# Kernel optimization log

Hardware: AMD Instinct MI355X
Metric: run time of the kernel (lower is better)

## Reference

```python
import jax, jax.numpy as jnp
import numpy as np

EPS = 1e-12
HEADS = 8
STRIDE = 4  # saccade_stride default

def conv1x1(x, w, b=None):
    # 1x1 conv == channel-mixing einsum; x: (B,C,H,W), w: (O,C)
    y = jnp.einsum('bchw,oc->bohw', x, w)
    if b is not None:
        y = y + b[None, :, None, None]
    return y

def ln2d(x, g, b, eps=1e-5):
    # LayerNorm across channel dim per spatial location (population variance)
    mu = x.mean(axis=1, keepdims=True)
    var = x.var(axis=1, keepdims=True)
    xn = (x - mu) / jnp.sqrt(var + eps)
    return xn * g[None, :, None, None] + b[None, :, None, None]

def l2norm(x):
    n = jnp.linalg.norm(x, axis=-1, keepdims=True)
    return x / jnp.maximum(n, EPS)

def cos_attn(q, k, v, scale):
    # q:(B,h,Q,d) k,v:(B,h,K,d); QK-normalized (cosine) attention
    logits = jnp.einsum('bhqd,bhkd->bhqk', l2norm(q), l2norm(k)) * scale
    a = jax.nn.softmax(logits, axis=-1)
    return jnp.einsum('bhqk,bhkd->bhqd', a, v)

def gqa(x, qkv_w, proj_w, proj_b):
    # grouped-query attention; group loop == per-head full attention
    B, C, H, W = x.shape
    hd = C // HEADS
    seq = H * W
    qkv = conv1x1(x, qkv_w).reshape(B, 3, HEADS, hd, seq)
    q, k, v = (jnp.swapaxes(qkv[:, i], -1, -2) for i in range(3))  # (B,h,seq,hd)
    out = cos_attn(q, k, v, hd ** -0.5)
    out = jnp.swapaxes(out, -1, -2).reshape(B, C, H, W)
    return conv1x1(out, proj_w, proj_b)

def block_forward(x, g1, b1, loc_qkv_w, loc_proj_w, loc_proj_b,
                  glob_qkv_w, glob_proj_w, glob_proj_b,
                  fuse_w1, fuse_b1, fuse_w2, fuse_b2,
                  glat, blat, latents, qlat_w, kvx_w, qx_w, kvlat_w,
                  lat_proj_w, lat_proj_b, g2, b2,
                  ffn_w1, ffn_b1, ffn_w2, ffn_b2):
    B, C, H, W = x.shape
    hd = C // HEADS
    seq = H * W
    scale = hd ** -0.5
    # --- BioAttentionFusion branch ---
    xn = ln2d(x, g1, b1)
    local = gqa(xn, loc_qkv_w, loc_proj_w, loc_proj_b)
    xc = xn.reshape(B, C, H // STRIDE, STRIDE, W // STRIDE, STRIDE).mean(axis=(3, 5))
    g = gqa(xc, glob_qkv_w, glob_proj_w, glob_proj_b)
    g = jax.image.resize(g, (B, C, H, W), method='bilinear')  # align_corners=False semantics
    f = conv1x1(jnp.concatenate([local, g], axis=1), fuse_w1, fuse_b1)
    f = conv1x1(jax.nn.gelu(f, approximate=False), fuse_w2, fuse_b2)
    x = x + f
    # --- LatentMixer branch ---
    xn = ln2d(x, glat, blat)
    L = latents.shape[-1]
    lat = jnp.broadcast_to(latents, (B, C, 1, L))
    ql = jnp.swapaxes(conv1x1(lat, qlat_w).reshape(B, HEADS, hd, L), -1, -2)
    kx, vx = jnp.split(conv1x1(xn, kvx_w), 2, axis=1)
    kx = jnp.swapaxes(kx.reshape(B, HEADS, hd, seq), -1, -2)
    vx = jnp.swapaxes(vx.reshape(B, HEADS, hd, seq), -1, -2)
    lat_read = cos_attn(ql, kx, vx, scale)  # latents read features
    lat_read = jnp.swapaxes(lat_read, -1, -2).reshape(B, C, 1, L)
    qx = jnp.swapaxes(conv1x1(xn, qx_w).reshape(B, HEADS, hd, seq), -1, -2)
    kl, vl = jnp.split(conv1x1(lat_read, kvlat_w), 2, axis=1)
    kl = jnp.swapaxes(kl.reshape(B, HEADS, hd, L), -1, -2)
    vl = jnp.swapaxes(vl.reshape(B, HEADS, hd, L), -1, -2)
    xw = cos_attn(qx, kl, vl, scale)  # features read latents back
    xw = jnp.swapaxes(xw, -1, -2).reshape(B, C, H, W)
    x = x + conv1x1(xw, lat_proj_w, lat_proj_b)
    # --- FFN branch ---
    xn = ln2d(x, g2, b2)
    h = jax.nn.gelu(conv1x1(xn, ffn_w1, ffn_b1), approximate=False)
    return x + conv1x1(h, ffn_w2, ffn_b2)

def setup_inputs() -> dict:
    key = jax.random.key(0)
    ks = jax.random.split(key, 24)
    B, C, H, W, L = 2, 128, 48, 48, 16
    def w(k, shape, s=0.02):
        return jax.random.normal(k, shape, jnp.float32) * s
    return {
        'x': jax.random.normal(ks[0], (B, C, H, W), jnp.float32),
        'g1': jnp.ones((C,), jnp.float32), 'b1': jnp.zeros((C,), jnp.float32),
        'loc_qkv_w': w(ks[1], (3 * C, C)),
        'loc_proj_w': w(ks[2], (C, C)), 'loc_proj_b': jnp.zeros((C,), jnp.float32),
        'glob_qkv_w': w(ks[3], (3 * C, C)),
        'glob_proj_w': w(ks[4], (C, C)), 'glob_proj_b': jnp.zeros((C,), jnp.float32),
        'fuse_w1': w(ks[5], (C, 2 * C)), 'fuse_b1': jnp.zeros((C,), jnp.float32),
        'fuse_w2': w(ks[6], (C, C)), 'fuse_b2': jnp.zeros((C,), jnp.float32),
        'glat': jnp.ones((C,), jnp.float32), 'blat': jnp.zeros((C,), jnp.float32),
        'latents': w(ks[7], (1, C, 1, L), 0.02),
        'qlat_w': w(ks[8], (C, C)), 'kvx_w': w(ks[9], (2 * C, C)),
        'qx_w': w(ks[10], (C, C)), 'kvlat_w': w(ks[11], (2 * C, C)),
        'lat_proj_w': w(ks[12], (C, C)), 'lat_proj_b': jnp.zeros((C,), jnp.float32),
        'g2': jnp.ones((C,), jnp.float32), 'b2': jnp.zeros((C,), jnp.float32),
        'ffn_w1': w(ks[13], (4 * C, C)), 'ffn_b1': jnp.zeros((4 * C,), jnp.float32),
        'ffn_w2': w(ks[14], (C, 4 * C)), 'ffn_b2': jnp.zeros((C,), jnp.float32),
    }

def reference(x, g1, b1, loc_qkv_w, loc_proj_w, loc_proj_b,
              glob_qkv_w, glob_proj_w, glob_proj_b,
              fuse_w1, fuse_b1, fuse_w2, fuse_b2,
              glat, blat, latents, qlat_w, kvx_w, qx_w, kvlat_w,
              lat_proj_w, lat_proj_b, g2, b2,
              ffn_w1, ffn_b1, ffn_w2, ffn_b2):
    return block_forward(x, g1, b1, loc_qkv_w, loc_proj_w, loc_proj_b,
                         glob_qkv_w, glob_proj_w, glob_proj_b,
                         fuse_w1, fuse_b1, fuse_w2, fuse_b2,
                         glat, blat, latents, qlat_w, kvx_w, qx_w, kvlat_w,
                         lat_proj_w, lat_proj_b, g2, b2,
                         ffn_w1, ffn_b1, ffn_w2, ffn_b2)
```

## Files before the change

kernel.cpp:

```cpp
#include <hip/hip_runtime.h>
#include <hip/hip_bf16.h>

typedef __hip_bfloat16 bf16;
typedef _Float16 f16;
typedef _Float16 f16x4 __attribute__((ext_vector_type(4)));
typedef float f32x4 __attribute__((ext_vector_type(4)));

#define HD 16
#define TK 128
#define KP 20
#define MINIT (-1e30f)

__device__ __forceinline__ float b2f(bf16 v){ return __bfloat162float(v); }
__device__ __forceinline__ float gelu_f(float x){ return 0.5f*x*(1.0f+erff(x*0.70710678118654752f)); }
__device__ __forceinline__ float rdv(const void* p, size_t i, bool bf){
  return bf ? b2f(((const bf16*)p)[i]) : ((const float*)p)[i];
}
__device__ __forceinline__ float4 ld4f(const void* p, size_t i, bool bf){
  if (bf){
    const bf16* q = (const bf16*)p + i;
    return make_float4(b2f(q[0]), b2f(q[1]), b2f(q[2]), b2f(q[3]));
  }
  return *(const float4*)((const float*)p + i);
}

__global__ void detect_k(const void* __restrict__ x, float* __restrict__ flag){
  if (blockIdx.x != 0) return;
  int l = threadIdx.x;
  const float* xf = (const float*)x;
  const bf16*  xb = (const bf16*)x;
  float sF = 0.f, sB = 0.f;
  for (int i = l; i < 512; i += 64){ float v = fabsf(xf[i]);      if (!(v < 1e30f)) v = 1e30f; sF += v; }
  for (int i = l; i < 1024; i += 64){ float v = fabsf(b2f(xb[i])); if (!(v < 1e30f)) v = 1e30f; sB += v; }
  #pragma unroll
  for (int o = 32; o; o >>= 1){ sF += __shfl_xor(sF, o); sB += __shfl_xor(sB, o); }
  if (l == 0){
    float mF = sF/512.f, mB = sB/1024.f;
    float dF = fabsf(logf(fmaxf(mF, 1e-30f)));
    float dB = fabsf(logf(fmaxf(mB, 1e-30f)));
    *flag = (dB <= dF) ? 1.0f : 0.0f;
  }
}

__global__ void cvt_k(const void* __restrict__ in, float* __restrict__ out, int n,
                      const float* __restrict__ flagp){
  bool bf = *flagp > 0.5f;
  int i = blockIdx.x*blockDim.x + threadIdx.x;
  if (i < n) out[i] = rdv(in, i, bf);
}

__global__ __launch_bounds__(256) void ln2dw_k(
    const float* __restrict__ x, const void* __restrict__ g,
    const void* __restrict__ b, float* __restrict__ y,
    int C, int HW, const float* __restrict__ flagp)
{
  __shared__ float redS[16][16];
  __shared__ float redQ[16][16];
  bool bf = *flagp > 0.5f;
  int t = threadIdx.x, pix = t & 15, sub = t >> 4;
  int p  = blockIdx.x*16 + pix;
  int bb = blockIdx.y;
  const float* xb = x + (size_t)bb*C*HW + p;
  float xv[8];
  float s = 0.f, s2 = 0.f;
  #pragma unroll
  for (int i = 0; i < 8; i++){
    float v = xb[(size_t)(sub*8 + i)*HW];
    xv[i] = v; s += v; s2 += v*v;
  }
  redS[sub][pix] = s; redQ[sub][pix] = s2;
  __syncthreads();
  float st = 0.f, qt = 0.f;
  #pragma unroll
  for (int j = 0; j < 16; j++){ st += redS[j][pix]; qt += redQ[j][pix]; }
  float mu  = st / (float)C;
  float var = fmaxf(qt / (float)C - mu*mu, 0.f);
  float inv = rsqrtf(var + 1e-5f);
  float* yb = y + (size_t)bb*C*HW + p;
  #pragma unroll
  for (int i = 0; i < 8; i++){
    int c = sub*8 + i;
    yb[(size_t)c*HW] = (xv[i] - mu)*inv*rdv(g, c, bf) + rdv(b, c, bf);
  }
}

__global__ void normk_k(float* __restrict__ KV, long kbs, int koff, int NK){
  int p = blockIdx.x*blockDim.x + threadIdx.x;
  if (p >= NK) return;
  int h = blockIdx.y, bb = blockIdx.z;
  float* base = KV + (size_t)bb*kbs + (size_t)(koff + h*16)*NK + p;
  float v[16]; float s = 0.f;
  #pragma unroll
  for (int d = 0; d < 16; d++){ v[d] = base[(size_t)d*NK]; s += v[d]*v[d]; }
  float iv = 1.f / fmaxf(sqrtf(s), 1e-12f);
  #pragma unroll
  for (int d = 0; d < 16; d++) base[(size_t)d*NK] = v[d]*iv;
}

__global__ void conv1x1_k(const float* __restrict__ in1, long in1_bs, int C1,
                          const float* __restrict__ in2, long in2_bs, int C2,
                          const void* __restrict__ w, const void* __restrict__ bias,
                          const float* __restrict__ res,
                          void* __restrict__ out, int to_out, int O, int NP, int act,
                          int raw1, const float* __restrict__ flagp){
  bool bf = *flagp > 0.5f;
  int p = blockIdx.x*blockDim.x + threadIdx.x;
  if (p >= NP) return;
  int o = blockIdx.y, bb = blockIdx.z;
  size_t wrow = (size_t)o*(C1 + C2);
  float acc = bias ? rdv(bias, o, bf) : 0.f;
  if (raw1){
    for (int c = 0; c < C1; c++)
      acc += rdv(w, wrow + c, bf) * rdv(in1, (size_t)bb*in1_bs + (size_t)c*NP + p, bf);
  } else {
    const float* i1 = in1 + (size_t)bb*in1_bs + p;
    for (int c = 0; c < C1; c++) acc += rdv(w, wrow + c, bf) * i1[(size_t)c*NP];
  }
  if (in2){
    const float* i2 = in2 + (size_t)bb*in2_bs + p;
    for (int c = 0; c < C2; c++) acc += rdv(w, wrow + C1 + c, bf) * i2[(size_t)c*NP];
  }
  if (act == 1) acc = gelu_f(acc);
  if (res) acc += res[((size_t)bb*O + o)*NP + p];
  size_t oi = ((size_t)bb*O + o)*NP + p;
  if (to_out){
    if (bf) ((bf16*)out)[oi] = __float2bfloat16(acc);
    else    ((float*)out)[oi] = acc;
  } else {
    ((float*)out)[oi] = acc;
  }
}

__global__ __launch_bounds__(64) void convmfma_k(
    const float* __restrict__ in1, long in1_bs, int C1,
    const float* __restrict__ in2, long in2_bs, int C2,
    const void* __restrict__ w, const void* __restrict__ bias,
    const float* __restrict__ res, void* __restrict__ out, int to_out,
    int O, int NP, int act, int nlo, int nhi, const float* __restrict__ flagp)
{
  bool bf = *flagp > 0.5f;
  int lane = threadIdx.x;
  int lm = lane & 15, lg = lane >> 4;
  int p0 = blockIdx.x*16, o0 = blockIdx.y*16, bb = blockIdx.z;
  int CW = C1 + C2;
  f32x4 d; d[0]=0.f; d[1]=0.f; d[2]=0.f; d[3]=0.f;
  const float* x1 = in1 + (size_t)bb*in1_bs + p0 + lm;
  const float* x2 = in2 ? (in2 + (size_t)bb*in2_bs + p0 + lm) : nullptr;
  #pragma unroll 8
  for (int kc = 0; kc < CW; kc += 16){
    f16x4 xb;
    #pragma unroll
    for (int i = 0; i < 4; i++){
      int c = kc + lg*4 + i;
      float v = (c < C1) ? x1[(size_t)c*NP] : x2[(size_t)(c - C1)*NP];
      xb[i] = (f16)v;
    }
    float4 wv = ld4f(w, (size_t)(o0 + lm)*CW + kc + lg*4, bf);
    f16x4 wa; wa[0]=(f16)wv.x; wa[1]=(f16)wv.y; wa[2]=(f16)wv.z; wa[3]=(f16)wv.w;
    d = __builtin_amdgcn_mfma_f32_16x16x16f16(wa, xb, d, 0, 0, 0);
  }
  if (o0 >= nlo && o0 < nhi){
    float ss = d[0]*d[0] + d[1]*d[1] + d[2]*d[2] + d[3]*d[3];
    ss += __shfl_xor(ss, 16); ss += __shfl_xor(ss, 32);
    float iv = 1.f / fmaxf(sqrtf(ss), 1e-12f);
    d[0]*=iv; d[1]*=iv; d[2]*=iv; d[3]*=iv;
  }
  #pragma unroll
  for (int r = 0; r < 4; r++){
    int o = o0 + lg*4 + r;
    float v = d[r] + (bias ? rdv(bias, o, bf) : 0.f);
    if (act == 1) v = gelu_f(v);
    size_t oi = ((size_t)bb*O + o)*NP + p0 + lm;
    if (res) v += res[oi];
    if (to_out && bf) ((bf16*)out)[oi] = __float2bfloat16(v);
    else              ((float*)out)[oi] = v;
  }
}

__global__ __launch_bounds__(512) void flat_mfma_k(
    const float* __restrict__ Q, long qbs, int qoff,
    const float* __restrict__ KV, long kbs, int koff, int voff,
    float* __restrict__ Out, long obs, int NQ, int NK, float scale)
{
  __shared__ float OS[8*4*16*17];
  __shared__ float LS[8*4*16];
  int t = threadIdx.x, lane = t & 63, wv = t >> 6;
  int h = blockIdx.y, bb = blockIdx.z;
  int qb = blockIdx.x*64;
  int lm = lane & 15, lg = lane >> 4;
  const float* qp  = Q  + (size_t)bb*qbs;
  const float* kvb = KV + (size_t)bb*kbs;
  f16x4 qf[4];
  #pragma unroll
  for (int qt = 0; qt < 4; qt++){
    float qv[4]; float ss = 0.f;
    #pragma unroll
    for (int i = 0; i < 4; i++){
      qv[i] = qp[(size_t)(qoff + h*16 + lg*4 + i)*NQ + qb + qt*16 + lm];
      ss += qv[i]*qv[i];
    }
    ss += __shfl_xor(ss, 16); ss += __shfl_xor(ss, 32);
    float inv = scale / fmaxf(sqrtf(ss), 1e-12f);
    #pragma unroll
    for (int i = 0; i < 4; i++) qf[qt][i] = (f16)(qv[i]*inv);
  }
  f32x4 of[4];
  float ls[4];
  #pragma unroll
  for (int qt = 0; qt < 4; qt++){
    of[qt][0]=0.f; of[qt][1]=0.f; of[qt][2]=0.f; of[qt][3]=0.f; ls[qt]=0.f;
  }
  int chunk = NK >> 3;
  int p0 = wv*chunk, p1 = p0 + chunk;
  const float* kc = kvb + (size_t)(koff + h*16)*NK;
  const float* vc = kvb + (size_t)(voff + h*16)*NK;
  for (int pos = p0; pos < p1; pos += 16){
    f16x4 kf;
    #pragma unroll
    for (int i = 0; i < 4; i++)
      kf[i] = (f16)kc[(size_t)(lg*4 + i)*NK + pos + lm];
    float4 vvv = *(const float4*)&vc[(size_t)lm*NK + pos + lg*4];
    f16x4 vf; vf[0]=(f16)vvv.x; vf[1]=(f16)vvv.y; vf[2]=(f16)vvv.z; vf[3]=(f16)vvv.w;
    #pragma unroll
    for (int qt = 0; qt < 4; qt++){
      f32x4 s; s[0]=0.f; s[1]=0.f; s[2]=0.f; s[3]=0.f;
      s = __builtin_amdgcn_mfma_f32_16x16x16f16(kf, qf[qt], s, 0, 0, 0);
      f16x4 pf;
      #pragma unroll
      for (int r = 0; r < 4; r++){
        float pp = __expf(s[r]);
        ls[qt] += pp;
        pf[r] = (f16)pp;
      }
      of[qt] = __builtin_amdgcn_mfma_f32_16x16x16f16(vf, pf, of[qt], 0, 0, 0);
    }
  }
  #pragma unroll
  for (int qt = 0; qt < 4; qt++){
    ls[qt] += __shfl_xor(ls[qt], 16);
    ls[qt] += __shfl_xor(ls[qt], 32);
    #pragma unroll
    for (int r = 0; r < 4; r++)
      OS[((wv*4 + qt)*16 + lm)*17 + lg*4 + r] = of[qt][r];
    if (lg == 0) LS[(wv*4 + qt)*16 + lm] = ls[qt];
  }
  __syncthreads();
  #pragma unroll
  for (int rep = 0; rep < 2; rep++){
    int o = t + rep*512;
    int d = o >> 6, qq = o & 63;
    int qt = qq >> 4, q = qq & 15;
    float acc = 0.f, lsum = 0.f;
    #pragma unroll
    for (int w = 0; w < 8; w++){
      acc  += OS[((w*4 + qt)*16 + q)*17 + d];
      lsum += LS[(w*4 + qt)*16 + q];
    }
    Out[(size_t)bb*obs + (size_t)(h*16 + d)*NQ + qb + qq] = acc / fmaxf(lsum, 1e-30f);
  }
}

__global__ __launch_bounds__(256) void attn4_k(
    const float* __restrict__ Q, long qbs, int qoff,
    const float* __restrict__ KV, long kbs, int koff, int voff,
    float* __restrict__ Out, long obs, int NQ, int NK, float scale)
{
  __shared__ __align__(16) float Ks[TK*KP];
  __shared__ __align__(16) float Vs[TK*KP];
  int tid = threadIdx.x;
  int sub = tid & 3;
  int h = blockIdx.y, bb = blockIdx.z;
  int qi = blockIdx.x*64 + (tid >> 2);
  bool qv = qi < NQ;
  float qn[4] = {0,0,0,0}, acc[4] = {0,0,0,0};
  float l = 0.f;
  if (qv){
    float s = 0.f;
    #pragma unroll
    for (int j = 0; j < 4; j++){
      qn[j] = Q[(size_t)bb*qbs + (size_t)(qoff + h*16 + sub*4 + j)*NQ + qi];
      s += qn[j]*qn[j];
    }
    s += __shfl_xor(s, 1); s += __shfl_xor(s, 2);
    float inv = scale / fmaxf(sqrtf(s), 1e-12f);
    #pragma unroll
    for (int j = 0; j < 4; j++) qn[j] *= inv;
  }
  for (int k0 = 0; k0 < NK; k0 += TK){
    int lim = min(TK, NK - k0);
    for (int i = tid; i < 16*TK; i += 256){
      int pos = i & (TK-1), d = i >> 7;
      if (pos < lim){
        Ks[pos*KP + d] = KV[(size_t)bb*kbs + (size_t)(koff + h*16 + d)*NK + k0 + pos];
        Vs[pos*KP + d] = KV[(size_t)bb*kbs + (size_t)(voff + h*16 + d)*NK + k0 + pos];
      }
    }
    __syncthreads();
    for (int pos = 0; pos < lim; pos++){
      float4 k4 = *(const float4*)&Ks[pos*KP + sub*4];
      float dd = qn[0]*k4.x + qn[1]*k4.y + qn[2]*k4.z + qn[3]*k4.w;
      dd += __shfl_xor(dd, 1); dd += __shfl_xor(dd, 2);
      float pp = __expf(dd);
      l += pp;
      float4 v4 = *(const float4*)&Vs[pos*KP + sub*4];
      acc[0] += pp*v4.x;
      acc[1] += pp*v4.y;
      acc[2] += pp*v4.z;
      acc[3] += pp*v4.w;
    }
    __syncthreads();
  }
  if (qv){
    float li = 1.f / fmaxf(l, 1e-30f);
    #pragma unroll
    for (int j = 0; j < 4; j++)
      Out[(size_t)bb*obs + (size_t)(h*16 + sub*4 + j)*NQ + qi] = acc[j]*li;
  }
}

__global__ void latpart_k(const float* __restrict__ ql, const float* __restrict__ kvx,
                          long kbs, float* __restrict__ part, int NK, int S){
  int s = blockIdx.x, h = blockIdx.y, bb = blockIdx.z;
  int t = threadIdx.x;
  int q = t & 15, sub = (t >> 4) & 3;
  float qn[16]; float ss = 0.f;
  #pragma unroll
  for (int d = 0; d < 16; d++){
    qn[d] = ql[(size_t)bb*2048 + (size_t)(h*16+d)*16 + q];
    ss += qn[d]*qn[d];
  }
  float inv = 0.25f / fmaxf(sqrtf(ss), 1e-12f);
  #pragma unroll
  for (int d = 0; d < 16; d++) qn[d] *= inv;
  float l = 0.f, acc[16];
  #pragma unroll
  for (int d = 0; d < 16; d++) acc[d] = 0.f;
  int chunk = NK / S, c4 = chunk >> 2;
  int k0 = s*chunk + sub*c4, k1 = k0 + c4;
  const float* kb = kvx + (size_t)bb*kbs;
  for (int pos = k0; pos < k1; pos++){
    float dot = 0.f;
    #pragma unroll
    for (int d = 0; d < 16; d++) dot += qn[d]*kb[(size_t)(h*16+d)*NK + pos];
    float pp = __expf(dot);
    l += pp;
    #pragma unroll
    for (int d = 0; d < 16; d++)
      acc[d] += pp*kb[(size_t)(128 + h*16+d)*NK + pos];
  }
  l += __shfl_xor(l, 16); l += __shfl_xor(l, 32);
  #pragma unroll
  for (int d = 0; d < 16; d++){
    acc[d] += __shfl_xor(acc[d], 16);
    acc[d] += __shfl_xor(acc[d], 32);
  }
  if ((t >> 4) == 0){
    size_t idx = (size_t)((((bb*8 + h)*16 + q)*S) + s)*18;
    part[idx] = l;
    #pragma unroll
    for (int d = 0; d < 16; d++) part[idx+1+d] = acc[d];
  }
}

__global__ void latcomb_k(const float* __restrict__ part, float* __restrict__ latr, int S){
  int i = blockIdx.x*blockDim.x + threadIdx.x;
  int d = i & 15, q = (i >> 4) & 15, h = (i >> 8) & 7, bb = i >> 11;
  size_t base = (size_t)(((bb*8 + h)*16 + q)*S)*18;
  float L = 0.f, a = 0.f;
  for (int s = 0; s < S; s++){
    const float* ps = part + base + (size_t)s*18;
    L += ps[0];
    a += ps[1+d];
  }
  latr[(size_t)bb*2048 + (size_t)(h*16+d)*16 + q] = a / fmaxf(L, 1e-30f);
}

__global__ void pool4_k(const float* __restrict__ xn, float* __restrict__ xc){
  int i = blockIdx.x*blockDim.x + threadIdx.x;
  if (i >= 2*128*144) return;
  int pc = i % 144; int bc = i / 144;
  int hc = pc / 12, wc = pc % 12;
  const float* s = xn + (size_t)bc*2304 + hc*4*48 + wc*4;
  float acc = 0.f;
  #pragma unroll
  for (int r = 0; r < 4; r++)
    #pragma unroll
    for (int c2 = 0; c2 < 4; c2++) acc += s[r*48 + c2];
  xc[i] = acc * 0.0625f;
}

__global__ void ups_k(const float* __restrict__ g, float* __restrict__ out){
  int i = blockIdx.x*blockDim.x + threadIdx.x;
  if (i >= 2*128*2304) return;
  int p = i % 2304; int bc = i / 2304;
  int h = p / 48, w = p % 48;
  float sh = h*0.25f - 0.375f;
  float sw = w*0.25f - 0.375f;
  float fh0 = floorf(sh), fw0 = floorf(sw);
  float fh = sh - fh0, fw = sw - fw0;
  int h0 = (int)fh0, w0 = (int)fw0;
  int h0c = min(11, max(0, h0)),   h1c = min(11, max(0, h0+1));
  int w0c = min(11, max(0, w0)),   w1c = min(11, max(0, w0+1));
  const float* s = g + (size_t)bc*144;
  float v00 = s[h0c*12 + w0c], v01 = s[h0c*12 + w1c];
  float v10 = s[h1c*12 + w0c], v11 = s[h1c*12 + w1c];
  out[i] = (1.f-fh)*((1.f-fw)*v00 + fw*v01) + fh*((1.f-fw)*v10 + fw*v11);
}

extern "C" void kernel_launch(void* const* d_in, const int* in_sizes, int n_in,
                              void* d_out, int out_size, void* d_ws, size_t ws_size,
                              hipStream_t stream){
  const int B = 2, C = 128, HW = 2304;
  const void* x_in        = d_in[0];
  const void* g1          = d_in[1];
  const void* b1          = d_in[2];
  const void* loc_qkv_w   = d_in[3];
  const void* loc_proj_w  = d_in[4];
  const void* loc_proj_b  = d_in[5];
  const void* glob_qkv_w  = d_in[6];
  const void* glob_proj_w = d_in[7];
  const void* glob_proj_b = d_in[8];
  const void* fuse_w1     = d_in[9];
  const void* fuse_b1     = d_in[10];
  const void* fuse_w2     = d_in[11];
  const void* fuse_b2     = d_in[12];
  const void* glat        = d_in[13];
  const void* blat        = d_in[14];
  const void* latents     = d_in[15];
  const void* qlat_w      = d_in[16];
  const void* kvx_w       = d_in[17];
  const void* qx_w        = d_in[18];
  const void* kvlat_w     = d_in[19];
  const void* lat_proj_w  = d_in[20];
  const void* lat_proj_b  = d_in[21];
  const void* g2          = d_in[22];
  const void* b2          = d_in[23];
  const void* ffn_w1      = d_in[24];
  const void* ffn_b1      = d_in[25];
  const void* ffn_w2      = d_in[26];
  const void* ffn_b2      = d_in[27];

  float* ws = (float*)d_ws;
  float* P  = ws + 0;
  float* N  = ws + 589824;
  float* A  = ws + 1179648;
  float* Q  = ws + 1769472;
  float* FLAG = ws + 4128768;

  float* qkv   = Q;
  float* L     = Q + 1769472;
  float* xc    = Q;
  float* qkvc  = Q + 36864;
  float* gatt  = Q + 147456;
  float* gproj = Q + 184320;
  float* kvx   = Q;
  float* qlat  = Q + 1181696;
  float* latr  = Q + 1185792;
  float* kvlat = Q + 1189888;
  float* part  = Q + 1198080;
  float* ffh   = Q;

  dim3 blk(256);
  dim3 blk512(512);
  dim3 blk64(64);

  detect_k<<<1, 64, 0, stream>>>(x_in, FLAG);
  cvt_k<<<2304, blk, 0, stream>>>(x_in, P, 589824, FLAG);

  ln2dw_k<<<dim3(144,B), blk, 0, stream>>>(P, g1, b1, N, C, HW, FLAG);
  convmfma_k<<<dim3(144,24,B), blk64, 0, stream>>>(N,(long)C*HW,C, nullptr,0,0, loc_qkv_w,nullptr,nullptr, qkv,0,384,HW,0, 128,256, FLAG);
  flat_mfma_k<<<dim3(36,8,B), blk512, 0, stream>>>(qkv,(long)384*HW,0, qkv,(long)384*HW,128,256, A,(long)C*HW, HW,HW,0.25f);
  convmfma_k<<<dim3(144,8,B), blk64, 0, stream>>>(A,(long)C*HW,C, nullptr,0,0, loc_proj_w,loc_proj_b,nullptr, L,0,C,HW,0, 0,0, FLAG);
  pool4_k<<<144, blk, 0, stream>>>(N, xc);
  conv1x1_k<<<dim3(1,384,B), blk, 0, stream>>>(xc,(long)C*144,C, nullptr,0,0, glob_qkv_w,nullptr,nullptr, qkvc,0,384,144,0, 0, FLAG);
  normk_k<<<dim3(1,8,B), blk, 0, stream>>>(qkvc, (long)384*144, 128, 144);
  attn4_k<<<dim3(3,8,B), blk, 0, stream>>>(qkvc,(long)384*144,0, qkvc,(long)384*144,128,256, gatt,(long)C*144, 144,144,0.25f);
  conv1x1_k<<<dim3(1,128,B), blk, 0, stream>>>(gatt,(long)C*144,C, nullptr,0,0, glob_proj_w,glob_proj_b,nullptr, gproj,0,C,144,0, 0, FLAG);
  ups_k<<<2304, blk, 0, stream>>>(gproj, A);
  convmfma_k<<<dim3(144,8,B), blk64, 0, stream>>>(L,(long)C*HW,C, A,(long)C*HW,C, fuse_w1,fuse_b1,nullptr, N,0,C,HW,1, 0,0, FLAG);
  convmfma_k<<<dim3(144,8,B), blk64, 0, stream>>>(N,(long)C*HW,C, nullptr,0,0, fuse_w2,fuse_b2,P, P,0,C,HW,0, 0,0, FLAG);

  ln2dw_k<<<dim3(144,B), blk, 0, stream>>>(P, glat, blat, N, C, HW, FLAG);
  convmfma_k<<<dim3(144,16,B), blk64, 0, stream>>>(N,(long)C*HW,C, nullptr,0,0, kvx_w,nullptr,nullptr, kvx,0,256,HW,0, 0,128, FLAG);
  convmfma_k<<<dim3(144,8,B), blk64, 0, stream>>>(N,(long)C*HW,C, nullptr,0,0, qx_w,nullptr,nullptr, A,0,C,HW,0, 0,0, FLAG);
  conv1x1_k<<<dim3(1,128,B), blk, 0, stream>>>((const float*)latents,0L,C, nullptr,0,0, qlat_w,nullptr,nullptr, qlat,0,C,16,0, 1, FLAG);
  latpart_k<<<dim3(48,8,B), 64, 0, stream>>>(qlat, kvx, (long)256*HW, part, HW, 48);
  latcomb_k<<<16, blk, 0, stream>>>(part, latr, 48);
  conv1x1_k<<<dim3(1,256,B), blk, 0, stream>>>(latr,(long)C*16,C, nullptr,0,0, kvlat_w,nullptr,nullptr, kvlat,0,256,16,0, 0, FLAG);
  normk_k<<<dim3(1,8,B), blk, 0, stream>>>(kvlat, (long)256*16, 0, 16);
  attn4_k<<<dim3(36,8,B), blk, 0, stream>>>(A,(long)C*HW,0, kvlat,(long)256*16,0,128, N,(long)C*HW, HW,16,0.25f);
  convmfma_k<<<dim3(144,8,B), blk64, 0, stream>>>(N,(long)C*HW,C, nullptr,0,0, lat_proj_w,lat_proj_b,P, P,0,C,HW,0, 0,0, FLAG);

  ln2dw_k<<<dim3(144,B), blk, 0, stream>>>(P, g2, b2, N, C, HW, FLAG);
  convmfma_k<<<dim3(144,32,B), blk64, 0, stream>>>(N,(long)C*HW,C, nullptr,0,0, ffn_w1,ffn_b1,nullptr, ffh,0,512,HW,1, 0,0, FLAG);
  convmfma_k<<<dim3(144,8,B), blk64, 0, stream>>>(ffh,(long)512*HW,512, nullptr,0,0, ffn_w2,ffn_b2,P, d_out,1,C,HW,0, 0,0, FLAG);
}
```

Measured before the change: 462.7 us.

## Fuse layernorm, pooling, upsample and k-norm into MFMA conv kernel

Extends the MFMA 1x1-conv kernel with optional prologues: a per-pixel channel layernorm computed via lane shuffles, 4x4 average pooling of the input, and bilinear upsampling of the second input. It also routes the small global and latent convolutions through the MFMA kernel, using its built-in L2-normalisation of the key rows. Together this removes the separate ln2d, pool, upsample, normk and scalar conv launches and their intermediate buffers. In exchange, the layernorm statistics are recomputed in every output-channel block (up to 32 times for the FFN), the pooling reads 16 values per input element, and the unroll factor drops to 4.

```diff
diff --git a/kernel.cpp b/kernel.cpp
--- a/kernel.cpp
+++ b/kernel.cpp
@@ -82,19 +82,6 @@
     int c = sub*8 + i;
     yb[(size_t)c*HW] = (xv[i] - mu)*inv*rdv(g, c, bf) + rdv(b, c, bf);
   }
-}
-
-__global__ void normk_k(float* __restrict__ KV, long kbs, int koff, int NK){
-  int p = blockIdx.x*blockDim.x + threadIdx.x;
-  if (p >= NK) return;
-  int h = blockIdx.y, bb = blockIdx.z;
-  float* base = KV + (size_t)bb*kbs + (size_t)(koff + h*16)*NK + p;
-  float v[16]; float s = 0.f;
-  #pragma unroll
-  for (int d = 0; d < 16; d++){ v[d] = base[(size_t)d*NK]; s += v[d]*v[d]; }
-  float iv = 1.f / fmaxf(sqrtf(s), 1e-12f);
-  #pragma unroll
-  for (int d = 0; d < 16; d++) base[(size_t)d*NK] = v[d]*iv;
 }
 
 __global__ void conv1x1_k(const float* __restrict__ in1, long in1_bs, int C1,
@@ -136,23 +123,71 @@
     const float* __restrict__ in2, long in2_bs, int C2,
     const void* __restrict__ w, const void* __restrict__ bias,
     const float* __restrict__ res, void* __restrict__ out, int to_out,
-    int O, int NP, int act, int nlo, int nhi, const float* __restrict__ flagp)
+    int O, int NP, int act, int nlo, int nhi,
+    int lnf, const void* __restrict__ lng, const void* __restrict__ lnb,
+    int pool, int ups2, const float* __restrict__ flagp)
 {
   bool bf = *flagp > 0.5f;
   int lane = threadIdx.x;
   int lm = lane & 15, lg = lane >> 4;
   int p0 = blockIdx.x*16, o0 = blockIdx.y*16, bb = blockIdx.z;
   int CW = C1 + C2;
+  const float* x1 = in1 + (size_t)bb*in1_bs + p0 + lm;
+  const float* x2b = in2 ? (in2 + (size_t)bb*in2_bs) : nullptr;
+  float fh = 0.f, fw = 0.f; int i00=0, i01=0, i10=0, i11=0;
+  if (ups2){
+    int p = p0 + lm; int hh = p/48, ww = p%48;
+    float sh = hh*0.25f - 0.375f, sw = ww*0.25f - 0.375f;
+    float fh0 = floorf(sh), fw0 = floorf(sw);
+    fh = sh - fh0; fw = sw - fw0;
+    int h0 = (int)fh0, w0 = (int)fw0;
+    int h0c = min(11, max(0, h0)), h1c = min(11, max(0, h0+1));
+    int w0c = min(11, max(0, w0)), w1c = min(11, max(0, w0+1));
+    i00 = h0c*12 + w0c; i01 = h0c*12 + w1c; i10 = h1c*12 + w0c; i11 = h1c*12 + w1c;
+  }
+  const float* pN = nullptr;
+  if (pool){
+    int pc = p0 + lm; int hc = pc/12, wc = pc%12;
+    pN = in1 + (size_t)bb*in1_bs + hc*192 + wc*4;
+  }
+  float mu = 0.f, linv = 0.f;
+  if (lnf){
+    float s = 0.f, s2 = 0.f;
+    for (int c = lg; c < CW; c += 4){ float v = x1[(size_t)c*NP]; s += v; s2 += v*v; }
+    s  += __shfl_xor(s, 16);  s  += __shfl_xor(s, 32);
+    s2 += __shfl_xor(s2, 16); s2 += __shfl_xor(s2, 32);
+    mu = s / (float)CW;
+    float var = fmaxf(s2/(float)CW - mu*mu, 0.f);
+    linv = rsqrtf(var + 1e-5f);
+  }
   f32x4 d; d[0]=0.f; d[1]=0.f; d[2]=0.f; d[3]=0.f;
-  const float* x1 = in1 + (size_t)bb*in1_bs + p0 + lm;
-  const float* x2 = in2 ? (in2 + (size_t)bb*in2_bs + p0 + lm) : nullptr;
-  #pragma unroll 8
+  #pragma unroll 4
   for (int kc = 0; kc < CW; kc += 16){
     f16x4 xb;
     #pragma unroll
     for (int i = 0; i < 4; i++){
       int c = kc + lg*4 + i;
-      float v = (c < C1) ? x1[(size_t)c*NP] : x2[(size_t)(c - C1)*NP];
+      float v;
+      if (pool){
+        const float* s = pN + (size_t)c*2304;
+        float a = 0.f;
+        #pragma unroll
+        for (int r = 0; r < 4; r++)
+          #pragma unroll
+          for (int cc = 0; cc < 4; cc++) a += s[r*48 + cc];
+        v = a * 0.0625f;
+      } else if (c < C1){
+        v = x1[(size_t)c*NP];
+        if (lnf) v = (v - mu)*linv*rdv(lng, c, bf) + rdv(lnb, c, bf);
+      } else {
+        int c2 = c - C1;
+        if (ups2){
+          const float* s = x2b + (size_t)c2*144;
+          v = (1.f-fh)*((1.f-fw)*s[i00] + fw*s[i01]) + fh*((1.f-fw)*s[i10] + fw*s[i11]);
+        } else {
+          v = x2b[(size_t)c2*NP + p0 + lm];
+        }
+      }
       xb[i] = (f16)v;
     }
     float4 wv = ld4f(w, (size_t)(o0 + lm)*CW + kc + lg*4, bf);
@@ -373,38 +408,6 @@
     a += ps[1+d];
   }
   latr[(size_t)bb*2048 + (size_t)(h*16+d)*16 + q] = a / fmaxf(L, 1e-30f);
-}
-
-__global__ void pool4_k(const float* __restrict__ xn, float* __restrict__ xc){
-  int i = blockIdx.x*blockDim.x + threadIdx.x;
-  if (i >= 2*128*144) return;
-  int pc = i % 144; int bc = i / 144;
-  int hc = pc / 12, wc = pc % 12;
-  const float* s = xn + (size_t)bc*2304 + hc*4*48 + wc*4;
-  float acc = 0.f;
-  #pragma unroll
-  for (int r = 0; r < 4; r++)
-    #pragma unroll
-    for (int c2 = 0; c2 < 4; c2++) acc += s[r*48 + c2];
-  xc[i] = acc * 0.0625f;
-}
-
-__global__ void ups_k(const float* __restrict__ g, float* __restrict__ out){
-  int i = blockIdx.x*blockDim.x + threadIdx.x;
-  if (i >= 2*128*2304) return;
-  int p = i % 2304; int bc = i / 2304;
-  int h = p / 48, w = p % 48;
-  float sh = h*0.25f - 0.375f;
-  float sw = w*0.25f - 0.375f;
-  float fh0 = floorf(sh), fw0 = floorf(sw);
-  float fh = sh - fh0, fw = sw - fw0;
-  int h0 = (int)fh0, w0 = (int)fw0;
-  int h0c = min(11, max(0, h0)),   h1c = min(11, max(0, h0+1));
-  int w0c = min(11, max(0, w0)),   w1c = min(11, max(0, w0+1));
-  const float* s = g + (size_t)bc*144;
-  float v00 = s[h0c*12 + w0c], v01 = s[h0c*12 + w1c];
-  float v10 = s[h1c*12 + w0c], v11 = s[h1c*12 + w1c];
-  out[i] = (1.f-fh)*((1.f-fw)*v00 + fw*v01) + fh*((1.f-fw)*v10 + fw*v11);
 }
 
 extern "C" void kernel_launch(void* const* d_in, const int* in_sizes, int n_in,
@@ -449,7 +452,6 @@
 
   float* qkv   = Q;
   float* L     = Q + 1769472;
-  float* xc    = Q;
   float* qkvc  = Q + 36864;
   float* gatt  = Q + 147456;
   float* gproj = Q + 184320;
@@ -468,30 +470,24 @@
   cvt_k<<<2304, blk, 0, stream>>>(x_in, P, 589824, FLAG);
 
   ln2dw_k<<<dim3(144,B), blk, 0, stream>>>(P, g1, b1, N, C, HW, FLAG);
-  convmfma_k<<<dim3(144,24,B), blk64, 0, stream>>>(N,(long)C*HW,C, nullptr,0,0, loc_qkv_w,nullptr,nullptr, qkv,0,384,HW,0, 128,256, FLAG);
+  convmfma_k<<<dim3(144,24,B), blk64, 0, stream>>>(N,(long)C*HW,C, nullptr,0,0, loc_qkv_w,nullptr,nullptr, qkv,0,384,HW,0, 128,256, 0,nullptr,nullptr, 0,0, FLAG);
   flat_mfma_k<<<dim3(36,8,B), blk512, 0, stream>>>(qkv,(long)384*HW,0, qkv,(long)384*HW,128,256, A,(long)C*HW, HW,HW,0.25f);
-  convmfma_k<<<dim3(144,8,B), blk64, 0, stream>>>(A,(long)C*HW,C, nullptr,0,0, loc_proj_w,loc_proj_b,nullptr, L,0,C,HW,0, 0,0, FLAG);
-  pool4_k<<<144, blk, 0, stream>>>(N, xc);
-  conv1x1_k<<<dim3(1,384,B), blk, 0, stream>>>(xc,(long)C*144,C, nullptr,0,0, glob_qkv_w,nullptr,nullptr, qkvc,0,384,144,0, 0, FLAG);
-  normk_k<<<dim3(1,8,B), blk, 0, stream>>>(qkvc, (long)384*144, 128, 144);
+  convmfma_k<<<dim3(144,8,B), blk64, 0, stream>>>(A,(long)C*HW,C, nullptr,0,0, loc_proj_w,loc_proj_b,nullptr, L,0,C,HW,0, 0,0, 0,nullptr,nullptr, 0,0, FLAG);
+  convmfma_k<<<dim3(9,24,B), blk64, 0, stream>>>(N,(long)C*HW,C, nullptr,0,0, glob_qkv_w,nullptr,nullptr, qkvc,0,384,144,0, 128,256, 0,nullptr,nullptr, 1,0, FLAG);
   attn4_k<<<dim3(3,8,B), blk, 0, stream>>>(qkvc,(long)384*144,0, qkvc,(long)384*144,128,256, gatt,(long)C*144, 144,144,0.25f);
-  conv1x1_k<<<dim3(1,128,B), blk, 0, stream>>>(gatt,(long)C*144,C, nullptr,0,0, glob_proj_w,glob_proj_b,nullptr, gproj,0,C,144,0, 0, FLAG);
-  ups_k<<<2304, blk, 0, stream>>>(gproj, A);
-  convmfma_k<<<dim3(144,8,B), blk64, 0, stream>>>(L,(long)C*HW,C, A,(long)C*HW,C, fuse_w1,fuse_b1,nullptr, N,0,C,HW,1, 0,0, FLAG);
-  convmfma_k<<<dim3(144,8,B), blk64, 0, stream>>>(N,(long)C*HW,C, nullptr,0,0, fuse_w2,fuse_b2,P, P,0,C,HW,0, 0,0, FLAG);
-
-  ln2dw_k<<<dim3(144,B), blk, 0, stream>>>(P, glat, blat, N, C, HW, FLAG);
-  convmfma_k<<<dim3(144,16,B), blk64, 0, stream>>>(N,(long)C*HW,C, nullptr,0,0, kvx_w,nullptr,nullptr, kvx,0,256,HW,0, 0,128, FLAG);
-  convmfma_k<<<dim3(144,8,B), blk64, 0, stream>>>(N,(long)C*HW,C, nullptr,0,0, qx_w,nullptr,nullptr, A,0,C,HW,0, 0,0, FLAG);
+  convmfma_k<<<dim3(9,8,B), blk64, 0, stream>>>(gatt,(long)C*144,C, nullptr,0,0, glob_proj_w,glob_proj_b,nullptr, gproj,0,C,144,0, 0,0, 0,nullptr,nullptr, 0,0, FLAG);
+  convmfma_k<<<dim3(144,8,B), blk64, 0, stream>>>(L,(long)C*HW,C, gproj,(long)C*144,C, fuse_w1,fuse_b1,nullptr, N,0,C,HW,1, 0,0, 0,nullptr,nullptr, 0,1, FLAG);
+  convmfma_k<<<dim3(144,8,B), blk64, 0, stream>>>(N,(long)C*HW,C, nullptr,0,0, fuse_w2,fuse_b2,P, P,0,C,HW,0, 0,0, 0,nullptr,nullptr, 0,0, FLAG);
+
+  convmfma_k<<<dim3(144,16,B), blk64, 0, stream>>>(P,(long)C*HW,C, nullptr,0,0, kvx_w,nullptr,nullptr, kvx,0,256,HW,0, 0,128, 1,glat,blat, 0,0, FLAG);
+  convmfma_k<<<dim3(144,8,B), blk64, 0, stream>>>(P,(long)C*HW,C, nullptr,0,0, qx_w,nullptr,nullptr, A,0,C,HW,0, 0,0, 1,glat,blat, 0,0, FLAG);
   conv1x1_k<<<dim3(1,128,B), blk, 0, stream>>>((const float*)latents,0L,C, nullptr,0,0, qlat_w,nullptr,nullptr, qlat,0,C,16,0, 1, FLAG);
   latpart_k<<<dim3(48,8,B), 64, 0, stream>>>(qlat, kvx, (long)256*HW, part, HW, 48);
   latcomb_k<<<16, blk, 0, stream>>>(part, latr, 48);
-  conv1x1_k<<<dim3(1,256,B), blk, 0, stream>>>(latr,(long)C*16,C, nullptr,0,0, kvlat_w,nullptr,nullptr, kvlat,0,256,16,0, 0, FLAG);
-  normk_k<<<dim3(1,8,B), blk, 0, stream>>>(kvlat, (long)256*16, 0, 16);
+  convmfma_k<<<dim3(1,16,B), blk64, 0, stream>>>(latr,(long)C*16,C, nullptr,0,0, kvlat_w,nullptr,nullptr, kvlat,0,256,16,0, 0,128, 0,nullptr,nullptr, 0,0, FLAG);
   attn4_k<<<dim3(36,8,B), blk, 0, stream>>>(A,(long)C*HW,0, kvlat,(long)256*16,0,128, N,(long)C*HW, HW,16,0.25f);
-  convmfma_k<<<dim3(144,8,B), blk64, 0, stream>>>(N,(long)C*HW,C, nullptr,0,0, lat_proj_w,lat_proj_b,P, P,0,C,HW,0, 0,0, FLAG);
-
-  ln2dw_k<<<dim3(144,B), blk, 0, stream>>>(P, g2, b2, N, C, HW, FLAG);
-  convmfma_k<<<dim3(144,32,B), blk64, 0, stream>>>(N,(long)C*HW,C, nullptr,0,0, ffn_w1,ffn_b1,nullptr, ffh,0,512,HW,1, 0,0, FLAG);
-  convmfma_k<<<dim3(144,8,B), blk64, 0, stream>>>(ffh,(long)512*HW,512, nullptr,0,0, ffn_w2,ffn_b2,P, d_out,1,C,HW,0, 0,0, FLAG);
-}
+  convmfma_k<<<dim3(144,8,B), blk64, 0, stream>>>(N,(long)C*HW,C, nullptr,0,0, lat_proj_w,lat_proj_b,P, P,0,C,HW,0, 0,0, 0,nullptr,nullptr, 0,0, FLAG);
+
+  convmfma_k<<<dim3(144,32,B), blk64, 0, stream>>>(P,(long)C*HW,C, nullptr,0,0, ffn_w1,ffn_b1,nullptr, ffh,0,512,HW,1, 0,0, 1,g2,b2, 0,0, FLAG);
+  convmfma_k<<<dim3(144,8,B), blk64, 0, stream>>>(ffh,(long)512*HW,512, nullptr,0,0, ffn_w2,ffn_b2,P, d_out,1,C,HW,0, 0,0, 0,nullptr,nullptr, 0,0, FLAG);
+}
```

Measured after the change: 438.0 us. -5.3%, faster.
